# Optimization experiments

Measured on AMD Instinct MI355X. Metric: run time of the kernel, lower is better.

## Reference

```python
import jax, jax.numpy as jnp
import numpy as np

N, H_IN, W_IN, D_OUT = 4, 512, 360, 512


def _ramp_filter(H):
    # fourier_fbp_filter(..., 'ramp') -> time domain, fftshifted, then reversed
    f = np.fft.fftfreq(H).reshape(-1, 1)
    fourier_filter = 2.0 * np.abs(f)
    time_filter = np.fft.fftshift(np.fft.ifft(fourier_filter, axis=0).real)
    time_filter = time_filter[::-1].copy()  # list-reverse in the original
    return time_filter.reshape(1, 1, H, 1).astype(np.float32)  # OIHW


def _backproj_ty(H, W, D):
    # y-coordinate of the grid_sample grid; x-coordinate exactly selects column i
    th = np.pi / 180.0 * np.linspace(0.0, 180.0, W, endpoint=False)  # [W]
    X, Y = np.mgrid[0:D, 0:D]
    xpr = (X - D // 2).astype(np.float64)
    ypr = (Y - D // 2).astype(np.float64)
    t = ypr[None] * np.cos(th)[:, None, None] - xpr[None] * np.sin(th)[:, None, None]
    return (t / (H // 2)).astype(np.float32)  # [W, D, D], in grid_sample coords


def setup_inputs() -> dict:
    key = jax.random.key(0)
    radon_image = jax.random.normal(key, (N, 1, H_IN, W_IN), dtype=jnp.float32)
    hG = jnp.asarray(_ramp_filter(H_IN))
    t_y = jnp.asarray(_backproj_ty(H_IN, W_IN, D_OUT))
    return {"radon_image": radon_image, "hG": hG, "t_y": t_y}


def _forward(radon_image, hG, t_y):
    Nb, _, H, W = radon_image.shape
    hH = H // 2
    padded = jnp.concatenate([radon_image, radon_image, radon_image], axis=2)  # [N,1,3H,W]
    filt = jax.lax.conv_general_dilated(
        padded, hG, window_strides=(1, 1), padding="VALID",
        dimension_numbers=("NCHW", "OIHW", "NCHW"))  # [N,1,2H+1,W]
    filt = filt[:, 0, hH + 1 : hH + H + 1, :]  # [N,H,W]

    cols = jnp.transpose(filt, (2, 0, 1))  # [W, N, H]: column i = angle i

    def body(acc, xs):
        col, ty = xs  # col: [N,H], ty: [D,D]
        # bilinear grid_sample along y, align_corners=True, zeros padding
        py = (ty + 1.0) * 0.5 * (H - 1)
        y0 = jnp.floor(py)
        fy = py - y0
        y0i = y0.astype(jnp.int32)
        y1i = y0i + 1
        w0 = jnp.where((y0i >= 0) & (y0i < H), 1.0 - fy, 0.0)
        w1 = jnp.where((y1i >= 0) & (y1i < H), fy, 0.0)
        v = col[:, jnp.clip(y0i, 0, H - 1)] * w0[None] \
          + col[:, jnp.clip(y1i, 0, H - 1)] * w1[None]  # [N,D,D]
        return acc + v, None

    D = t_y.shape[1]
    acc0 = jnp.zeros((Nb, D, D), dtype=filt.dtype)
    acc, _ = jax.lax.scan(body, acc0, (cols, t_y))
    return (acc * (np.pi / (2.0 * W)))[:, None]  # [N,1,D,D]


def reference(radon_image, hG, t_y):
    return _forward(radon_image, hG, t_y)
```

## Files before the change

kernel.cpp:

```cpp
#include <hip/hip_runtime.h>

#define HH 512
#define WW 360
#define NB 4
#define DD 512

#define NCHUNK 12
#define ANG_PER 30

#define OFF_TAB  0
#define OFF_RT   1024
#define OFF_FILT (1024 + NB*WW*HH)
#define OFF_PART (OFF_FILT + WW*HH*NB)
#define CHUNK_ELEMS (NB*DD*DD)

#define PAD    128
#define COLS_N 768

#define GLOAD_LDS16(gp, lp)                                                   \
    __builtin_amdgcn_global_load_lds(                                         \
        (const __attribute__((address_space(1))) void*)(gp),                  \
        (__attribute__((address_space(3))) void*)(lp), 16, 0, 0)

__global__ __launch_bounds__(256) void k_transpose(const float* __restrict__ radon,
                                                   float* __restrict__ ws) {
    __shared__ float tile[32][33];
    int n  = blockIdx.z;
    int w0 = blockIdx.x * 32, h0 = blockIdx.y * 32;
    int x = threadIdx.x, y = threadIdx.y;
    const float* rn = radon + n * (HH * WW);
#pragma unroll
    for (int r = 0; r < 32; r += 8) {
        int h = h0 + y + r, w = w0 + x;
        tile[y + r][x] = (w < WW) ? rn[h * WW + w] : 0.f;
    }
    __syncthreads();
    float* rt = ws + OFF_RT + n * (WW * HH);
#pragma unroll
    for (int r = 0; r < 32; r += 8) {
        int w = w0 + y + r, h = h0 + x;
        if (w < WW) rt[w * HH + h] = tile[x][y + r];
    }
}

__global__ __launch_bounds__(256) void k_filter(const float* __restrict__ hG,
                                                float* __restrict__ ws) {
    __shared__ float r2[NB][1024];
    int wA  = blockIdx.x;
    int tid = threadIdx.x;

    if (tid == 0) {
        double th = (3.14159265358979323846 / 180.0) * (0.5 * (double)wA);
        double c = cos(th), s = sin(th);
        float2 ab;
        ab.x = (float)(c * (255.5 / 256.0));
        ab.y = (float)(-s * (255.5 / 256.0));
        ((float2*)(ws + OFF_TAB))[wA] = ab;
    }

    const float* rt = ws + OFF_RT;
    for (int t = tid; t < NB * 1024; t += 256) {
        int n = t >> 10, i = t & 1023;
        r2[n][i] = rt[(n * WW + wA) * HH + ((i + 257) & 511)];
    }
    __syncthreads();

    int n = tid >> 6, lane = tid & 63, y0 = lane << 3;
    float acc[8] = {0, 0, 0, 0, 0, 0, 0, 0};
    const float* rr = &r2[n][y0];
    float4 Wr0 = *(const float4*)(rr + 0);
    float4 Wr1 = *(const float4*)(rr + 4);
    float4 Wr2 = *(const float4*)(rr + 8);
    float4 Wr3 = *(const float4*)(rr + 12);

    for (int d = 0; d < 512; d += 8) {
        float hg[8];
#pragma unroll
        for (int q = 0; q < 8; ++q) hg[q] = hG[d + q];
        float wf[16] = {Wr0.x, Wr0.y, Wr0.z, Wr0.w, Wr1.x, Wr1.y, Wr1.z, Wr1.w,
                        Wr2.x, Wr2.y, Wr2.z, Wr2.w, Wr3.x, Wr3.y, Wr3.z, Wr3.w};
#pragma unroll
        for (int du = 0; du < 8; ++du)
#pragma unroll
            for (int u = 0; u < 8; ++u)
                acc[u] = fmaf(wf[du + u], hg[du], acc[u]);
        if (d < 504) {
            Wr0 = Wr2; Wr1 = Wr3;
            Wr2 = *(const float4*)(rr + d + 16);
            Wr3 = *(const float4*)(rr + d + 20);
        }
    }
    float* filt = ws + OFF_FILT;
#pragma unroll
    for (int u = 0; u < 8; ++u)
        filt[(wA * HH + y0 + u) * NB + n] = acc[u];
}

__global__ __launch_bounds__(256, 6) void k_backproj(const float* __restrict__ ws,
                                                     float* __restrict__ parts) {
    __shared__ float4 cols[2][COLS_N];
    const int tid   = threadIdx.x;
    const int lane  = tid & 63;
    const int ithr  = tid >> 6;
    const int j     = blockIdx.x * 64 + lane;
    const int i0    = blockIdx.y * 32 + ithr;
    const int chunk = blockIdx.z;

    {
        int b = tid >> 7, r = tid & 127;
        float4 z = make_float4(0.f, 0.f, 0.f, 0.f);
        cols[b][r]            = z;
        cols[b][PAD + HH + r] = z;
    }

    const float2* tab = (const float2*)(ws + OFF_TAB);
    const float4* fd  = (const float4*)(ws + OFF_FILT);

    float acc[8][4];
#pragma unroll
    for (int u = 0; u < 8; ++u)
#pragma unroll
        for (int n = 0; n < 4; ++n) acc[u][n] = 0.f;

    float jf = (float)(j - 256);
    float ifl[8];
#pragma unroll
    for (int u = 0; u < 8; ++u) ifl[u] = (float)(i0 + 4 * u - 256);

    const int wbeg = chunk * ANG_PER;
    {
        const float4* src = fd + (size_t)wbeg * HH;
#pragma unroll
        for (int c = 0; c < 2; ++c) {
            int idx = tid + c * 256;
            GLOAD_LDS16(src + idx, &cols[0][PAD + idx]);
        }
    }
    __syncthreads();

    int cur = 0;
    for (int k = 0; k < ANG_PER; ++k) {
        const int w = wbeg + k;
        if (k + 1 < ANG_PER) {
            const float4* src = fd + (size_t)(w + 1) * HH;
            float4* dst = &cols[cur ^ 1][PAD];
#pragma unroll
            for (int c = 0; c < 2; ++c) {
                int idx = tid + c * 256;
                GLOAD_LDS16(src + idx, dst + idx);
            }
        }

        float2 ab = tab[w];
        float pybase = fmaf(ab.x, jf, 255.5f + (float)PAD);
        const float4* cb = cols[cur];
#pragma unroll
        for (int u = 0; u < 8; ++u) {
            float pyp = fmaf(ab.y, ifl[u], pybase);
            float cf  = truncf(pyp);
            float fy  = pyp - cf;
            int   c   = (int)cf;
            float4 p0 = cb[c];
            float4 p1 = cb[c + 1];
            float w0  = 1.f - fy;
            acc[u][0] = fmaf(p1.x, fy, fmaf(p0.x, w0, acc[u][0]));
            acc[u][1] = fmaf(p1.y, fy, fmaf(p0.y, w0, acc[u][1]));
            acc[u][2] = fmaf(p1.z, fy, fmaf(p0.z, w0, acc[u][2]));
            acc[u][3] = fmaf(p1.w, fy, fmaf(p0.w, w0, acc[u][3]));
        }
        __syncthreads();
        cur ^= 1;
    }

    float* part = parts + (size_t)chunk * CHUNK_ELEMS;
#pragma unroll
    for (int n = 0; n < 4; ++n)
#pragma unroll
        for (int u = 0; u < 8; ++u)
            part[(n * DD + (i0 + 4 * u)) * DD + j] = acc[u][n];
}

__global__ __launch_bounds__(256) void k_reduce(float* __restrict__ out,
                                                const float* __restrict__ ws) {
    int t = blockIdx.x * 256 + threadIdx.x;
    const float4* p = (const float4*)(ws + OFF_PART);
    const int C4 = CHUNK_ELEMS / 4;
    float4 a = p[t];
#pragma unroll
    for (int c = 1; c < NCHUNK; ++c) {
        float4 b = p[t + c * C4];
        a.x += b.x; a.y += b.y; a.z += b.z; a.w += b.w;
    }
    const float s = (float)(3.14159265358979323846 / 720.0);
    float4 r;
    r.x = a.x * s; r.y = a.y * s; r.z = a.z * s; r.w = a.w * s;
    ((float4*)out)[t] = r;
}

extern "C" void kernel_launch(void* const* d_in, const int* in_sizes, int n_in,
                              void* d_out, int out_size, void* d_ws, size_t ws_size,
                              hipStream_t stream) {
    const float* radon = (const float*)d_in[0];
    const float* hG    = (const float*)d_in[1];
    float* out = (float*)d_out;
    float* ws  = (float*)d_ws;

    k_transpose<<<dim3(12, 16, 4), dim3(32, 8), 0, stream>>>(radon, ws);
    k_filter<<<WW, 256, 0, stream>>>(hG, ws);
    k_backproj<<<dim3(8, 16, NCHUNK), 256, 0, stream>>>(ws, ws + OFF_PART);
    k_reduce<<<1024, 256, 0, stream>>>(out, ws);
}
```

Baseline: 107.4 us.

## Stage only the per-tile detector window into LDS in backprojection

Backprojection blocks now compute, for each angle, the minimum detector coordinate their 64x32 pixel tile touches. They then load only a 128-entry window of the filtered column into LDS instead of the whole padded 512-entry column. The filtered buffer is re-laid out with a 768-stride zero-padded row written by the filter kernel, so windows near the edges read zeros from global memory. This cuts global-to-LDS traffic and LDS footprint per block, which could raise occupancy, at the cost of extra per-angle bound arithmetic. It also assumes a tile's projection span fits within 128 entries.

```diff
diff --git a/kernel.cpp b/kernel.cpp
--- a/kernel.cpp
+++ b/kernel.cpp
@@ -8,14 +8,15 @@
 #define NCHUNK 12
 #define ANG_PER 30
 
+#define FSTRIDE 768
+#define FOFFS   128
+#define NR      128
+
 #define OFF_TAB  0
 #define OFF_RT   1024
 #define OFF_FILT (1024 + NB*WW*HH)
-#define OFF_PART (OFF_FILT + WW*HH*NB)
+#define OFF_PART (OFF_FILT + (WW+1)*FSTRIDE*4)
 #define CHUNK_ELEMS (NB*DD*DD)
-
-#define PAD    128
-#define COLS_N 768
 
 #define GLOAD_LDS16(gp, lp)                                                   \
     __builtin_amdgcn_global_load_lds(                                         \
@@ -57,6 +58,11 @@
         ab.y = (float)(-s * (255.5 / 256.0));
         ((float2*)(ws + OFF_TAB))[wA] = ab;
     }
+    {
+        float4* fp = (float4*)(ws + OFF_FILT) + (size_t)wA * FSTRIDE;
+        float4 z = make_float4(0.f, 0.f, 0.f, 0.f);
+        if (tid < 128) { fp[tid] = z; fp[640 + tid] = z; }
+    }
 
     const float* rt = ws + OFF_RT;
     for (int t = tid; t < NB * 1024; t += 256) {
@@ -93,12 +99,12 @@
     float* filt = ws + OFF_FILT;
 #pragma unroll
     for (int u = 0; u < 8; ++u)
-        filt[(wA * HH + y0 + u) * NB + n] = acc[u];
+        filt[((size_t)wA * FSTRIDE + FOFFS + y0 + u) * 4 + n] = acc[u];
 }
 
 __global__ __launch_bounds__(256, 6) void k_backproj(const float* __restrict__ ws,
                                                      float* __restrict__ parts) {
-    __shared__ float4 cols[2][COLS_N];
+    __shared__ float4 buf[2][NR];
     const int tid   = threadIdx.x;
     const int lane  = tid & 63;
     const int ithr  = tid >> 6;
@@ -106,13 +112,6 @@
     const int i0    = blockIdx.y * 32 + ithr;
     const int chunk = blockIdx.z;
 
-    {
-        int b = tid >> 7, r = tid & 127;
-        float4 z = make_float4(0.f, 0.f, 0.f, 0.f);
-        cols[b][r]            = z;
-        cols[b][PAD + HH + r] = z;
-    }
-
     const float2* tab = (const float2*)(ws + OFF_TAB);
     const float4* fd  = (const float4*)(ws + OFF_FILT);
 
@@ -127,38 +126,48 @@
 #pragma unroll
     for (int u = 0; u < 8; ++u) ifl[u] = (float)(i0 + 4 * u - 256);
 
+    const float jlo = (float)((int)blockIdx.x * 64 - 256);
+    const float jhi = (float)((int)blockIdx.x * 64 + 63 - 256);
+    const float ilo = (float)((int)blockIdx.y * 32 - 256);
+    const float ihi = (float)((int)blockIdx.y * 32 + 31 - 256);
+
     const int wbeg = chunk * ANG_PER;
+    float2 abc = tab[wbeg];
+    float2 abn = tab[wbeg + 1];
+
+    float basefc;
     {
-        const float4* src = fd + (size_t)wbeg * HH;
-#pragma unroll
-        for (int c = 0; c < 2; ++c) {
-            int idx = tid + c * 256;
-            GLOAD_LDS16(src + idx, &cols[0][PAD + idx]);
-        }
-    }
+        float t = fminf(fmaf(abc.x, jlo, 255.5f), fmaf(abc.x, jhi, 255.5f));
+        float pymin = fminf(fmaf(abc.y, ilo, t), fmaf(abc.y, ihi, t));
+        basefc = floorf(pymin) - 2.0f;
+    }
+    if (tid < NR)
+        GLOAD_LDS16(fd + (size_t)wbeg * FSTRIDE + (FOFFS + (int)basefc + tid),
+                    &buf[0][tid]);
     __syncthreads();
 
     int cur = 0;
     for (int k = 0; k < ANG_PER; ++k) {
         const int w = wbeg + k;
+        float2 abn2 = tab[min(w + 2, WW - 1)];
+        float basefn = 0.f;
         if (k + 1 < ANG_PER) {
-            const float4* src = fd + (size_t)(w + 1) * HH;
-            float4* dst = &cols[cur ^ 1][PAD];
-#pragma unroll
-            for (int c = 0; c < 2; ++c) {
-                int idx = tid + c * 256;
-                GLOAD_LDS16(src + idx, dst + idx);
-            }
+            float t = fminf(fmaf(abn.x, jlo, 255.5f), fmaf(abn.x, jhi, 255.5f));
+            float pymin = fminf(fmaf(abn.y, ilo, t), fmaf(abn.y, ihi, t));
+            basefn = floorf(pymin) - 2.0f;
+            if (tid < NR)
+                GLOAD_LDS16(fd + (size_t)(w + 1) * FSTRIDE + (FOFFS + (int)basefn + tid),
+                            &buf[cur ^ 1][tid]);
         }
 
-        float2 ab = tab[w];
-        float pybase = fmaf(ab.x, jf, 255.5f + (float)PAD);
-        const float4* cb = cols[cur];
+        float pybase = fmaf(abc.x, jf, 255.5f);
+        const float4* cb = buf[cur];
 #pragma unroll
         for (int u = 0; u < 8; ++u) {
-            float pyp = fmaf(ab.y, ifl[u], pybase);
-            float cf  = truncf(pyp);
-            float fy  = pyp - cf;
+            float pya = fmaf(abc.y, ifl[u], pybase);
+            float pyr = pya - basefc;
+            float cf  = truncf(pyr);
+            float fy  = pyr - cf;
             int   c   = (int)cf;
             float4 p0 = cb[c];
             float4 p1 = cb[c + 1];
@@ -169,7 +178,7 @@
             acc[u][3] = fmaf(p1.w, fy, fmaf(p0.w, w0, acc[u][3]));
         }
         __syncthreads();
-        cur ^= 1;
+        abc = abn; abn = abn2; basefc = basefn; cur ^= 1;
     }
 
     float* part = parts + (size_t)chunk * CHUNK_ELEMS;
```

Result: no change. 109.4 us (+1.8%).
